# Optimization experiments

Hardware: AMD Instinct MI355X
Metric: run time of the kernel (lower is better)

Reference implementation:

```python
import jax, jax.numpy as jnp
import numpy as np

HIDDEN = 1024
HEADS = 16
HEAD_DIM = HIDDEN // HEADS


def setup_inputs() -> dict:
    key = jax.random.key(0)
    ks = jax.random.split(key, 7)
    B, S = 4, 2048
    xav = float(np.sqrt(6.0 / (HIDDEN + HIDDEN)))  # xavier uniform bound
    def lin(k):
        return jax.random.uniform(k, (HIDDEN, HIDDEN), jnp.float32, -xav, xav)
    return {
        "hidden_states": jax.random.normal(ks[0], (B, S, HIDDEN), jnp.float32),
        "Wq": lin(ks[1]), "bq": jnp.zeros((HIDDEN,), jnp.float32),
        "Wk": lin(ks[2]), "bk": jnp.zeros((HIDDEN,), jnp.float32),
        "Wv": lin(ks[3]), "bv": jnp.zeros((HIDDEN,), jnp.float32),
    }


def reference(hidden_states, Wq, bq, Wk, bk, Wv, bv):
    B, S, H = hidden_states.shape
    def split_heads(t):  # [B,S,H] -> [B,heads,S,head_dim]
        return t.reshape(B, S, HEADS, HEAD_DIM).transpose(0, 2, 1, 3)
    q = split_heads(hidden_states @ Wq + bq)
    k = split_heads(hidden_states @ Wk + bk)
    v = split_heads(hidden_states @ Wv + bv)
    scores = jnp.einsum("bhqd,bhkd->bhqk", q, k) / jnp.sqrt(
        jnp.asarray(HEAD_DIM, hidden_states.dtype))
    probs = jax.nn.softmax(scores, axis=-1)  # dropout p=0.0 (inference)
    ctx = jnp.einsum("bhqk,bhkd->bhqd", probs, v)
    ctx = ctx.transpose(0, 2, 1, 3).reshape(B, S, H)
    return ctx
```

## Files before the change

### kernel.cpp

```cpp
#include <hip/hip_runtime.h>
#include <hip/hip_bf16.h>
#include <cstdint>

#define HIDDEN 1024
#define HEADS 16
#define HDIM 64
#define BATCH 4
#define SEQ 2048
#define MTOT (BATCH * SEQ)

typedef __attribute__((ext_vector_type(8))) short bfrag;
typedef __attribute__((ext_vector_type(4))) float cfrag;
typedef __attribute__((ext_vector_type(4))) float float4v;
typedef __attribute__((ext_vector_type(4))) unsigned short ushort4v;
typedef __attribute__((ext_vector_type(2))) unsigned int uint2v;

#define AS1 __attribute__((address_space(1)))
#define AS3 __attribute__((address_space(3)))

__device__ __forceinline__ void gl_lds16(const void* g, void* l) {
  __builtin_amdgcn_global_load_lds((AS1 void*)g, (AS3 void*)l, 16, 0, 0);
}

__device__ __forceinline__ uint16_t f2b(float f) {
  union { float f; uint32_t u; } v; v.f = f;
  uint32_t u = v.u;
  return (uint16_t)((u + 0x7FFFu + ((u >> 16) & 1u)) >> 16);
}

__global__ __launch_bounds__(256) void cvt_x_kernel(const float* __restrict__ in,
                                                    uint16_t* __restrict__ out, int n8) {
  int i = blockIdx.x * blockDim.x + threadIdx.x;
  if (i >= n8) return;
  float4v a = ((const float4v*)in)[2 * i];
  float4v b = ((const float4v*)in)[2 * i + 1];
  bfrag o;
  o[0] = (short)f2b(a[0]); o[1] = (short)f2b(a[1]);
  o[2] = (short)f2b(a[2]); o[3] = (short)f2b(a[3]);
  o[4] = (short)f2b(b[0]); o[5] = (short)f2b(b[1]);
  o[6] = (short)f2b(b[2]); o[7] = (short)f2b(b[3]);
  ((bfrag*)out)[i] = o;
}

__global__ __launch_bounds__(256) void cvt_w_kernel(const float* __restrict__ W0,
                                                    const float* __restrict__ W1,
                                                    const float* __restrict__ W2,
                                                    uint16_t* __restrict__ Wt) {
  const float* W = blockIdx.z == 0 ? W0 : (blockIdx.z == 1 ? W1 : W2);
  uint16_t* out = Wt + (size_t)blockIdx.z * HIDDEN * HIDDEN;
  __shared__ float tile[64][65];
  int n0 = blockIdx.x * 64, k0 = blockIdx.y * 64;
  int t = threadIdx.x;
  int r = t >> 2, cq = (t & 3) * 16;
#pragma unroll
  for (int i = 0; i < 16; i += 4) {
    float4v v = *(const float4v*)&W[(size_t)(k0 + r) * HIDDEN + n0 + cq + i];
    tile[r][cq + i + 0] = v[0]; tile[r][cq + i + 1] = v[1];
    tile[r][cq + i + 2] = v[2]; tile[r][cq + i + 3] = v[3];
  }
  __syncthreads();
  bfrag o0, o1;
#pragma unroll
  for (int i = 0; i < 8; ++i) o0[i] = (short)f2b(tile[cq + i][r]);
#pragma unroll
  for (int i = 0; i < 8; ++i) o1[i] = (short)f2b(tile[cq + 8 + i][r]);
  *(bfrag*)&out[(size_t)(n0 + r) * HIDDEN + k0 + cq] = o0;
  *(bfrag*)&out[(size_t)(n0 + r) * HIDDEN + k0 + cq + 8] = o1;
}

__global__ __launch_bounds__(256) void gemm_qkv_kernel(
    const uint16_t* __restrict__ X, const uint16_t* __restrict__ Wt,
    const float* __restrict__ b0, const float* __restrict__ b1,
    const float* __restrict__ b2,
    uint16_t* __restrict__ Qo, uint16_t* __restrict__ Ko, uint16_t* __restrict__ Vo) {
  __shared__ uint16_t As[128 * 32];
  __shared__ uint16_t Bs[128 * 32];
  int which = blockIdx.z;
  const uint16_t* Wp = Wt + (size_t)which * HIDDEN * HIDDEN;
  const float* bias = which == 0 ? b0 : (which == 1 ? b1 : b2);

  int m0 = blockIdx.x * 128, n0 = blockIdx.y * 128;
  int tid = threadIdx.x;
  int wave = tid >> 6, lane = tid & 63;
  int wm = wave >> 1, wn = wave & 1;
  int g = lane >> 4, c = lane & 15;
  int sr = lane >> 2;
  int sc = (lane & 3) * 8;

  cfrag acc[4][4];
#pragma unroll
  for (int i = 0; i < 4; ++i)
#pragma unroll
    for (int j = 0; j < 4; ++j) acc[i][j] = cfrag{0.f, 0.f, 0.f, 0.f};

  for (int kt = 0; kt < HIDDEN / 32; ++kt) {
    int kc = kt * 32 + sc;
#pragma unroll
    for (int i = 0; i < 2; ++i) {
      int rowA = (i * 4 + wave) * 16;
      gl_lds16(&X[(size_t)(m0 + rowA + sr) * HIDDEN + kc], &As[rowA * 32]);
      gl_lds16(&Wp[(size_t)(n0 + rowA + sr) * HIDDEN + kc], &Bs[rowA * 32]);
    }
    __syncthreads();
    bfrag af[4], bf[4];
#pragma unroll
    for (int mt = 0; mt < 4; ++mt)
      af[mt] = *(const bfrag*)&As[(wm * 64 + mt * 16 + c) * 32 + g * 8];
#pragma unroll
    for (int nt = 0; nt < 4; ++nt)
      bf[nt] = *(const bfrag*)&Bs[(wn * 64 + nt * 16 + c) * 32 + g * 8];
#pragma unroll
    for (int mt = 0; mt < 4; ++mt)
#pragma unroll
      for (int nt = 0; nt < 4; ++nt)
        acc[mt][nt] = __builtin_amdgcn_mfma_f32_16x16x32_bf16(af[mt], bf[nt],
                                                              acc[mt][nt], 0, 0, 0);
    __syncthreads();
  }

  if (which == 2) {
    int bb_ = m0 >> 11;
    int s0 = (m0 & 2047) + wm * 64;
#pragma unroll
    for (int nt = 0; nt < 4; ++nt) {
      int n = n0 + wn * 64 + nt * 16 + c;
      int h = n >> 6, d = n & 63;
      float bb = bias[n];
      size_t base = ((size_t)(bb_ * 16 + h) * 64 + d) * SEQ;
#pragma unroll
      for (int mt = 0; mt < 4; ++mt) {
        int s = s0 + mt * 16 + g * 4;
        ushort4v pk;
        pk[0] = f2b(acc[mt][nt][0] + bb);
        pk[1] = f2b(acc[mt][nt][1] + bb);
        pk[2] = f2b(acc[mt][nt][2] + bb);
        pk[3] = f2b(acc[mt][nt][3] + bb);
        *(ushort4v*)&Vo[base + s] = pk;
      }
    }
  } else {
    uint16_t* out = which == 0 ? Qo : Ko;
    float sc_ = which == 0 ? 0.125f : 1.0f;
#pragma unroll
    for (int nt = 0; nt < 4; ++nt) {
      int n = n0 + wn * 64 + nt * 16 + c;
      float bb = bias[n];
#pragma unroll
      for (int mt = 0; mt < 4; ++mt) {
        int mb = m0 + wm * 64 + mt * 16 + g * 4;
#pragma unroll
        for (int r = 0; r < 4; ++r)
          out[(size_t)(mb + r) * HIDDEN + n] = f2b((acc[mt][nt][r] + bb) * sc_);
      }
    }
  }
}

__global__ __launch_bounds__(256, 4) void attn_kernel(
    const uint16_t* __restrict__ Q, const uint16_t* __restrict__ K,
    const uint16_t* __restrict__ VT, float* __restrict__ out) {
  __shared__ uint16_t Ks[2][64 * 64];
  __shared__ uint16_t Vs[2][64 * 64];
  __shared__ __align__(16) uint16_t Pl[4][16][64];

  int bid = blockIdx.x;
  int wg = (bid & 7) * 256 + (bid >> 3);
  int bh = wg >> 5, qt = wg & 31;
  int b = bh >> 4, h = bh & 15;
  int tid = threadIdx.x, wave = tid >> 6, lane = tid & 63;
  int g = lane >> 4, c = lane & 15;
  size_t rowb = (size_t)b * SEQ;
  int colb = h * HDIM;
  const uint16_t* Kh = K + rowb * HIDDEN + colb;
  const uint16_t* Vh = VT + (size_t)bh * HDIM * SEQ;

  int r8 = lane >> 3, c8 = lane & 7;
  int scol = ((c8 ^ r8) << 3);
  int sbrow = (wave & 1) * 32;

  int qrow = qt * 64 + wave * 16 + c;
  bfrag aq[2];
  aq[0] = *(const bfrag*)&Q[(rowb + qrow) * HIDDEN + colb + g * 8];
  aq[1] = *(const bfrag*)&Q[(rowb + qrow) * HIDDEN + colb + 32 + g * 8];

  float mr = -INFINITY, lr = 0.f;
  cfrag oacc[4];
#pragma unroll
  for (int dt = 0; dt < 4; ++dt) oacc[dt] = cfrag{0.f, 0.f, 0.f, 0.f};

  if (wave < 2) {
#pragma unroll
    for (int j = 0; j < 4; ++j) {
      int rl = sbrow + j * 8;
      gl_lds16(&Kh[(size_t)(rl + r8) * HIDDEN + scol], &Ks[0][rl * 64]);
    }
  } else {
#pragma unroll
    for (int j = 0; j < 4; ++j) {
      int rl = sbrow + j * 8;
      gl_lds16(&Vh[(size_t)(rl + r8) * SEQ + scol], &Vs[0][rl * 64]);
    }
  }
  __syncthreads();

  int cur = 0;
  int sw = (c & 7) << 4;
  uint8_t* Pb = (uint8_t*)Pl + wave * 2048 + c * 128;

  for (int t = 0; t < 32; ++t) {
    int j0 = t * 64;
    if (t < 31) {
      int jn = j0 + 64;
      if (wave < 2) {
#pragma unroll
        for (int j = 0; j < 4; ++j) {
          int rl = sbrow + j * 8;
          gl_lds16(&Kh[(size_t)(jn + rl + r8) * HIDDEN + scol],
                   &Ks[cur ^ 1][rl * 64]);
        }
      } else {
#pragma unroll
        for (int j = 0; j < 4; ++j) {
          int rl = sbrow + j * 8;
          gl_lds16(&Vh[(size_t)(rl + r8) * SEQ + jn + scol],
                   &Vs[cur ^ 1][rl * 64]);
        }
      }
    }

    const uint8_t* Kbuf = (const uint8_t*)Ks[cur];
    const uint8_t* Vbuf = (const uint8_t*)Vs[cur];

    cfrag s[4];
#pragma unroll
    for (int nt = 0; nt < 4; ++nt) s[nt] = cfrag{0.f, 0.f, 0.f, 0.f};
    __builtin_amdgcn_s_setprio(1);
#pragma unroll
    for (int kb = 0; kb < 2; ++kb) {
#pragma unroll
      for (int nt = 0; nt < 4; ++nt) {
        int off = ((nt * 16 + c) * 128 + kb * 64 + g * 16) ^ sw;
        bfrag bk = *(const bfrag*)(Kbuf + off);
        s[nt] = __builtin_amdgcn_mfma_f32_16x16x32_bf16(bk, aq[kb], s[nt], 0, 0, 0);
      }
    }
    __builtin_amdgcn_s_setprio(0);

    float mx = fmaxf(fmaxf(s[0][0], s[0][1]), fmaxf(s[0][2], s[0][3]));
#pragma unroll
    for (int nt = 1; nt < 4; ++nt)
      mx = fmaxf(mx, fmaxf(fmaxf(s[nt][0], s[nt][1]), fmaxf(s[nt][2], s[nt][3])));
    mx = fmaxf(mx, __shfl_xor(mx, 16, 64));
    mx = fmaxf(mx, __shfl_xor(mx, 32, 64));
    if (mx > mr + 8.0f) {
      float alpha = __expf(mr - mx);
      lr *= alpha;
#pragma unroll
      for (int dt = 0; dt < 4; ++dt)
#pragma unroll
        for (int r = 0; r < 4; ++r) oacc[dt][r] *= alpha;
      mr = mx;
    }
    float ps = 0.f;
#pragma unroll
    for (int nt = 0; nt < 4; ++nt) {
#pragma unroll
      for (int r = 0; r < 4; ++r) s[nt][r] = __expf(s[nt][r] - mr);
      ps += (s[nt][0] + s[nt][1]) + (s[nt][2] + s[nt][3]);
    }
    ps += __shfl_xor(ps, 16, 64);
    ps += __shfl_xor(ps, 32, 64);
    lr += ps;

#pragma unroll
    for (int nt = 0; nt < 4; ++nt) {
      uint32_t w0, w1;
      asm("v_cvt_pk_bf16_f32 %0, %1, %2" : "=v"(w0) : "v"(s[nt][0]), "v"(s[nt][1]));
      asm("v_cvt_pk_bf16_f32 %0, %1, %2" : "=v"(w1) : "v"(s[nt][2]), "v"(s[nt][3]));
      uint2v pw; pw[0] = w0; pw[1] = w1;
      *(uint2v*)(Pb + ((nt * 32 + g * 8) ^ sw)) = pw;
    }
    asm volatile("s_waitcnt lgkmcnt(0)" ::: "memory");
    __builtin_amdgcn_sched_barrier(0);

    __builtin_amdgcn_s_setprio(1);
#pragma unroll
    for (int kb = 0; kb < 2; ++kb) {
      bfrag ap = *(const bfrag*)(Pb + ((kb * 64 + g * 16) ^ sw));
#pragma unroll
      for (int dt = 0; dt < 4; ++dt) {
        int off = ((dt * 16 + c) * 128 + kb * 64 + g * 16) ^ sw;
        bfrag bv = *(const bfrag*)(Vbuf + off);
        oacc[dt] = __builtin_amdgcn_mfma_f32_16x16x32_bf16(bv, ap, oacc[dt], 0, 0, 0);
      }
    }
    __builtin_amdgcn_s_setprio(0);

    __syncthreads();
    cur ^= 1;
  }

  float inv = 1.0f / lr;
  size_t orow = rowb + (size_t)qt * 64 + wave * 16 + c;
#pragma unroll
  for (int dt = 0; dt < 4; ++dt) {
    float4v o;
    o[0] = oacc[dt][0] * inv; o[1] = oacc[dt][1] * inv;
    o[2] = oacc[dt][2] * inv; o[3] = oacc[dt][3] * inv;
    *(float4v*)&out[orow * HIDDEN + colb + dt * 16 + g * 4] = o;
  }
}

extern "C" void kernel_launch(void* const* d_in, const int* in_sizes, int n_in,
                              void* d_out, int out_size, void* d_ws, size_t ws_size,
                              hipStream_t stream) {
  const float* x  = (const float*)d_in[0];
  const float* Wq = (const float*)d_in[1];
  const float* bq = (const float*)d_in[2];
  const float* Wk = (const float*)d_in[3];
  const float* bk = (const float*)d_in[4];
  const float* Wv = (const float*)d_in[5];
  const float* bv = (const float*)d_in[6];
  float* out = (float*)d_out;

  uint8_t* ws = (uint8_t*)d_ws;
  const size_t XB = 0;
  const size_t WT = XB + (size_t)MTOT * HIDDEN * 2;
  const size_t QB = WT + (size_t)3 * HIDDEN * HIDDEN * 2;
  const size_t KB = QB + (size_t)MTOT * HIDDEN * 2;
  const size_t VB = KB + (size_t)MTOT * HIDDEN * 2;
  uint16_t* Xb = (uint16_t*)(ws + XB);
  uint16_t* Wt = (uint16_t*)(ws + WT);
  uint16_t* Qb = (uint16_t*)(ws + QB);
  uint16_t* Kb = (uint16_t*)(ws + KB);
  uint16_t* Vb = (uint16_t*)(ws + VB);

  cvt_x_kernel<<<dim3(MTOT * HIDDEN / 8 / 256), 256, 0, stream>>>(x, Xb,
                                                                  MTOT * HIDDEN / 8);
  cvt_w_kernel<<<dim3(16, 16, 3), 256, 0, stream>>>(Wq, Wk, Wv, Wt);
  gemm_qkv_kernel<<<dim3(64, 8, 3), 256, 0, stream>>>(Xb, Wt, bq, bk, bv, Qb, Kb, Vb);
  attn_kernel<<<dim3(2048), 256, 0, stream>>>(Qb, Kb, Vb, out);
}
```

Before: 294.4 us.

## Use exp2 softmax with folded log2e, defer row-sum reduction, remap GEMM blocks per XCD

The Q scale now also includes log2(e), so the attention softmax can use the hardware exp2 instruction instead of __expf. The per-tile cross-lane reduction of the row sum moves out of the loop and runs once before normalisation. The explicit LDS waitcnt and sched_barrier before the PV MFMAs are removed, leaving that ordering to the compiler. The QKV GEMM launch becomes a flat 1D grid whose block index is remapped so blocks sharing rows of X land on the same XCD for L2 reuse. Together these cut transcendental and shuffle cost per tile and improve GEMM cache locality, with a small risk to scheduling or ordering from dropping the explicit barrier.

New measurement: 277.0 us. 1.06x faster.

```diff
diff --git a/kernel.cpp b/kernel.cpp
--- a/kernel.cpp
+++ b/kernel.cpp
@@ -75,11 +75,17 @@
     uint16_t* __restrict__ Qo, uint16_t* __restrict__ Ko, uint16_t* __restrict__ Vo) {
   __shared__ uint16_t As[128 * 32];
   __shared__ uint16_t Bs[128 * 32];
-  int which = blockIdx.z;
+
+  int id = blockIdx.x;
+  int xcd = id & 7, j = id >> 3;
+  int which = j >> 6;
+  int r_ = j & 63;
+  int m0 = (xcd * 8 + (r_ >> 3)) * 128;
+  int n0 = (r_ & 7) * 128;
+
   const uint16_t* Wp = Wt + (size_t)which * HIDDEN * HIDDEN;
   const float* bias = which == 0 ? b0 : (which == 1 ? b1 : b2);
 
-  int m0 = blockIdx.x * 128, n0 = blockIdx.y * 128;
   int tid = threadIdx.x;
   int wave = tid >> 6, lane = tid & 63;
   int wm = wave >> 1, wn = wave & 1;
@@ -91,7 +97,7 @@
 #pragma unroll
   for (int i = 0; i < 4; ++i)
 #pragma unroll
-    for (int j = 0; j < 4; ++j) acc[i][j] = cfrag{0.f, 0.f, 0.f, 0.f};
+    for (int jj = 0; jj < 4; ++jj) acc[i][jj] = cfrag{0.f, 0.f, 0.f, 0.f};
 
   for (int kt = 0; kt < HIDDEN / 32; ++kt) {
     int kc = kt * 32 + sc;
@@ -140,7 +146,7 @@
     }
   } else {
     uint16_t* out = which == 0 ? Qo : Ko;
-    float sc_ = which == 0 ? 0.125f : 1.0f;
+    float sc_ = which == 0 ? 0.125f * 1.44269504088896f : 1.0f;
 #pragma unroll
     for (int nt = 0; nt < 4; ++nt) {
       int n = n0 + wn * 64 + nt * 16 + c;
@@ -246,14 +252,15 @@
     }
     __builtin_amdgcn_s_setprio(0);
 
-    float mx = fmaxf(fmaxf(s[0][0], s[0][1]), fmaxf(s[0][2], s[0][3]));
-#pragma unroll
-    for (int nt = 1; nt < 4; ++nt)
-      mx = fmaxf(mx, fmaxf(fmaxf(s[nt][0], s[nt][1]), fmaxf(s[nt][2], s[nt][3])));
+    float mx = fmaxf(fmaxf(fmaxf(s[0][0], s[0][1]), s[0][2]), s[0][3]);
+    float mx1 = fmaxf(fmaxf(fmaxf(s[1][0], s[1][1]), s[1][2]), s[1][3]);
+    float mx2 = fmaxf(fmaxf(fmaxf(s[2][0], s[2][1]), s[2][2]), s[2][3]);
+    float mx3 = fmaxf(fmaxf(fmaxf(s[3][0], s[3][1]), s[3][2]), s[3][3]);
+    mx = fmaxf(fmaxf(mx, mx1), fmaxf(mx2, mx3));
     mx = fmaxf(mx, __shfl_xor(mx, 16, 64));
     mx = fmaxf(mx, __shfl_xor(mx, 32, 64));
     if (mx > mr + 8.0f) {
-      float alpha = __expf(mr - mx);
+      float alpha = __builtin_amdgcn_exp2f(mr - mx);
       lr *= alpha;
 #pragma unroll
       for (int dt = 0; dt < 4; ++dt)
@@ -265,11 +272,10 @@
 #pragma unroll
     for (int nt = 0; nt < 4; ++nt) {
 #pragma unroll
-      for (int r = 0; r < 4; ++r) s[nt][r] = __expf(s[nt][r] - mr);
+      for (int r = 0; r < 4; ++r)
+        s[nt][r] = __builtin_amdgcn_exp2f(s[nt][r] - mr);
       ps += (s[nt][0] + s[nt][1]) + (s[nt][2] + s[nt][3]);
     }
-    ps += __shfl_xor(ps, 16, 64);
-    ps += __shfl_xor(ps, 32, 64);
     lr += ps;
 
 #pragma unroll
@@ -280,8 +286,6 @@
       uint2v pw; pw[0] = w0; pw[1] = w1;
       *(uint2v*)(Pb + ((nt * 32 + g * 8) ^ sw)) = pw;
     }
-    asm volatile("s_waitcnt lgkmcnt(0)" ::: "memory");
-    __builtin_amdgcn_sched_barrier(0);
 
     __builtin_amdgcn_s_setprio(1);
 #pragma unroll
@@ -300,6 +304,8 @@
     cur ^= 1;
   }
 
+  lr += __shfl_xor(lr, 16, 64);
+  lr += __shfl_xor(lr, 32, 64);
   float inv = 1.0f / lr;
   size_t orow = rowb + (size_t)qt * 64 + wave * 16 + c;
 #pragma unroll
@@ -338,6 +344,6 @@
   cvt_x_kernel<<<dim3(MTOT * HIDDEN / 8 / 256), 256, 0, stream>>>(x, Xb,
                                                                   MTOT * HIDDEN / 8);
   cvt_w_kernel<<<dim3(16, 16, 3), 256, 0, stream>>>(Wq, Wk, Wv, Wt);
-  gemm_qkv_kernel<<<dim3(64, 8, 3), 256, 0, stream>>>(Xb, Wt, bq, bk, bv, Qb, Kb, Vb);
+  gemm_qkv_kernel<<<dim3(1536), 256, 0, stream>>>(Xb, Wt, bq, bk, bv, Qb, Kb, Vb);
   attn_kernel<<<dim3(2048), 256, 0, stream>>>(Qb, Kb, Vb, out);
 }
```
